# Kernel tuning notes

Hardware: AMD Instinct MI355X
Metric: run time of the kernel (lower is better)

The kernel has to match this reference:

```python
import jax, jax.numpy as jnp
import numpy as np

B, S, D = 2, 1024, 1024
E = 8          # routed experts
I = 1024       # per-expert intermediate
IS = 1024      # shared expert intermediate
TOP_K = 2
NUM_SHARED = 1


def setup_inputs() -> dict:
    key = jax.random.key(0)
    ks = jax.random.split(key, 8)
    scale = 0.02
    return {
        "x": jax.random.normal(ks[0], (B, S, D), dtype=jnp.float32),
        "w_gate": jax.random.normal(ks[1], (D, E), dtype=jnp.float32) * scale,
        "wg": jax.random.normal(ks[2], (E, D, I), dtype=jnp.float32) * scale,  # expert gate_proj
        "wu": jax.random.normal(ks[3], (E, D, I), dtype=jnp.float32) * scale,  # expert up_proj
        "wd": jax.random.normal(ks[4], (E, I, D), dtype=jnp.float32) * scale,  # expert down_proj
        "ws_g": jax.random.normal(ks[5], (NUM_SHARED, D, IS), dtype=jnp.float32) * scale,
        "ws_u": jax.random.normal(ks[6], (NUM_SHARED, D, IS), dtype=jnp.float32) * scale,
        "ws_d": jax.random.normal(ks[7], (NUM_SHARED, IS, D), dtype=jnp.float32) * scale,
    }


def _swiglu(t, w_gate_proj, w_up, w_down):
    # t: [N, D]
    g = t @ w_gate_proj            # [N, I]
    u = t @ w_up                   # [N, I]
    return (jax.nn.silu(g) * u) @ w_down  # [N, D]


def reference(x, w_gate, wg, wu, wd, ws_g, ws_u, ws_d):
    Bb, Ss, Dd = x.shape
    x_flat = x.reshape(Bb * Ss, Dd)                  # [N, D]
    N = x_flat.shape[0]

    # --- router ---
    logits = x_flat @ w_gate                          # [N, E]
    topk_logits, topk_idx = jax.lax.top_k(logits, TOP_K)
    topk_w = jax.nn.softmax(topk_logits, axis=-1)     # [N, K]

    # --- aux load-balancing loss ---
    one_hot = jax.nn.one_hot(topk_idx, E, dtype=jnp.float32)  # [N, K, E]
    f = one_hot.sum(axis=1).mean(axis=0)                       # [E]
    P = jax.nn.softmax(logits, axis=-1).mean(axis=0)           # [E]
    aux_loss = E * jnp.sum(f * P)

    # --- combine weights: cw[n, e] = sum_k topk_w[n,k] * 1[topk_idx[n,k]==e] ---
    cw = jnp.einsum("nk,nke->ne", topk_w, one_hot)             # [N, E]

    # --- routed experts: dense compute over all experts, weighted combine ---
    g = jnp.einsum("nd,edi->eni", x_flat, wg)                  # [E, N, I]
    u = jnp.einsum("nd,edi->eni", x_flat, wu)                  # [E, N, I]
    a = jax.nn.silu(g) * u                                     # [E, N, I]
    y = jnp.einsum("eni,eid->end", a, wd)                      # [E, N, D]
    routed = jnp.einsum("ne,end->nd", cw, y)                   # [N, D]

    # --- shared experts ---
    shared = jnp.zeros_like(x_flat)
    for s in range(NUM_SHARED):
        shared = shared + _swiglu(x_flat, ws_g[s], ws_u[s], ws_d[s])

    out = (routed + shared).reshape(Bb, Ss, Dd)
    return out, aux_loss
```

## Files before the change

kernel.cpp:

```cpp
#include <hip/hip_runtime.h>
#include <math.h>

typedef unsigned short u16;
typedef __attribute__((ext_vector_type(8))) short short8;
typedef __attribute__((ext_vector_type(4))) float f32x4;
typedef __attribute__((ext_vector_type(4))) unsigned short u16x4;
typedef __attribute__((ext_vector_type(8))) unsigned short u16x8;

#define N_TOK 2048
#define DIM 1024
#define OUT_ELEMS 2097152

#define GLDS16(gp, lp) __builtin_amdgcn_global_load_lds( \
    (const __attribute__((address_space(1))) unsigned int*)(gp), \
    (__attribute__((address_space(3))) unsigned int*)(lp), 16, 0, 0)

__device__ __forceinline__ u16 f2bf(float f) {
    union { float f; unsigned u; } v; v.f = f;
    unsigned r = (v.u + 0x7FFFu + ((v.u >> 16) & 1u)) >> 16;
    return (u16)r;
}
__device__ __forceinline__ float bf2f(u16 h) {
    union { unsigned u; float f; } v; v.u = ((unsigned)h) << 16;
    return v.f;
}

__device__ __forceinline__ void cvt_chunk(const float* __restrict__ src,
                                          u16* __restrict__ dst, int chunk,
                                          char* smem, int t) {
    float* tile = (float*)smem;
    const char* gsrc = (const char*)(src + (size_t)chunk * 8192);
    u16* dchunk = dst + (size_t)chunk * 8192;
    int w = t >> 6, l = t & 63;
#pragma unroll
    for (int j = 0; j < 8; j++) {
        int idx = w * 8 + j;
        GLDS16(gsrc + idx * 1024 + l * 16, smem + idx * 1024);
    }
    __syncthreads();
    int n0 = (t & 63) * 4 + (t >> 6) * 256;
    f32x4 v[8];
#pragma unroll
    for (int k = 0; k < 8; k++)
        v[k] = *(const f32x4*)(tile + k * 1024 + n0);
#pragma unroll
    for (int i = 0; i < 4; i++) {
        u16x8 o;
#pragma unroll
        for (int k = 0; k < 8; k++) o[k] = f2bf(v[k][i]);
        *(u16x8*)(dchunk + (size_t)(n0 + i) * 8) = o;
    }
}

__global__ __launch_bounds__(256)
void k_front(const float* __restrict__ wg, const float* __restrict__ wu,
             const float* __restrict__ wsg, const float* __restrict__ wsu,
             u16* __restrict__ wgt, u16* __restrict__ wut,
             u16* __restrict__ wsgt, u16* __restrict__ wsut,
             const float* __restrict__ x, const float* __restrict__ wgate,
             u16* __restrict__ xb, int* __restrict__ tidx, float* __restrict__ tw,
             float* __restrict__ Pp, int* __restrict__ Cp,
             int* __restrict__ tlist, int* __restrict__ curs) {
    __shared__ __attribute__((aligned(128))) char smem[32768];
    int bx = blockIdx.x;
    int t = threadIdx.x;
    if (bx < 2304) {
        int mat = bx >> 7, chunk = bx & 127;
        const float* src; u16* dst;
        if      (mat <  8) { src = wg + (size_t)mat * 1048576;       dst = wgt + (size_t)mat * 1048576; }
        else if (mat < 16) { src = wu + (size_t)(mat - 8) * 1048576; dst = wut + (size_t)(mat - 8) * 1048576; }
        else if (mat == 16){ src = wsg; dst = wsgt; }
        else               { src = wsu; dst = wsut; }
        cvt_chunk(src, dst, chunk, smem, t);
        return;
    }
    int b = bx - 2304;
    float* sP = (float*)smem;
    int*   sC = (int*)(smem + 64);
    if (t < 8) { sP[t] = 0.f; sC[t] = 0; }
    if (b == 0 && t < 16) curs[t] = 0;
    __syncthreads();
    int wave = t >> 6;
    int lane = t & 63;
    int n = b * 4 + wave;
    const float* xr = x + (size_t)n * DIM;
    u16* xbr = xb + (size_t)n * DIM;
    float acc[8] = {0.f,0.f,0.f,0.f,0.f,0.f,0.f,0.f};
#pragma unroll
    for (int i = 0; i < 16; i++) {
        int d = lane + i * 64;
        float xv = xr[d];
        xbr[d] = f2bf(xv);
        const float* wr = wgate + d * 8;
#pragma unroll
        for (int e = 0; e < 8; e++) acc[e] += xv * wr[e];
    }
#pragma unroll
    for (int off = 32; off; off >>= 1) {
#pragma unroll
        for (int e = 0; e < 8; e++) acc[e] += __shfl_xor(acc[e], off);
    }
    if (lane == 0) {
        tlist[4096 + n] = n;
        float mx = acc[0];
#pragma unroll
        for (int e = 1; e < 8; e++) mx = fmaxf(mx, acc[e]);
        float p[8], s = 0.f;
#pragma unroll
        for (int e = 0; e < 8; e++) { p[e] = expf(acc[e] - mx); s += p[e]; }
        float inv = 1.f / s;
#pragma unroll
        for (int e = 0; e < 8; e++) atomicAdd(&sP[e], p[e] * inv);
        int i0 = 0; float b0 = acc[0];
#pragma unroll
        for (int e = 1; e < 8; e++) if (acc[e] > b0) { b0 = acc[e]; i0 = e; }
        int i1 = -1; float b1 = -3.4e38f;
#pragma unroll
        for (int e = 0; e < 8; e++) if (e != i0 && acc[e] > b1) { b1 = acc[e]; i1 = e; }
        float w0 = 1.f / (1.f + expf(b1 - b0));
        tidx[n * 2] = i0; tidx[n * 2 + 1] = i1;
        tw[n * 2] = w0;   tw[n * 2 + 1] = 1.f - w0;
        atomicAdd(&sC[i0], 1);
        atomicAdd(&sC[i1], 1);
    }
    __syncthreads();
    if (t < 8) { Pp[b * 8 + t] = sP[t]; Cp[b * 8 + t] = sC[t]; }
}

__global__ void k_scatter(const int* __restrict__ tidx, const float* __restrict__ Pp,
                          const int* __restrict__ Cp, int* __restrict__ curs,
                          int* __restrict__ tlist, int* __restrict__ slots,
                          float* __restrict__ out, int* __restrict__ counts,
                          int* __restrict__ offs) {
    __shared__ int   s_off[8];
    __shared__ int   sCnt[8];
    __shared__ float sPs[8];
    __shared__ int   redC[256];
    __shared__ float redP[256];
    int t = threadIdx.x;
    int e = t & 7, g = t >> 3;
    int cs = 0; float ps = 0.f;
#pragma unroll
    for (int j = 0; j < 16; j++) {
        int b = g + j * 32;
        cs += Cp[b * 8 + e];
        ps += Pp[b * 8 + e];
    }
    redC[t] = cs; redP[t] = ps;
    __syncthreads();
    if (t < 8) {
        int c = 0; float p = 0.f;
        for (int g2 = 0; g2 < 32; g2++) { c += redC[g2 * 8 + t]; p += redP[g2 * 8 + t]; }
        sCnt[t] = c; sPs[t] = p;
    }
    __syncthreads();
    if (t == 0) {
        int o = 0;
        for (int e2 = 0; e2 < 8; e2++) { s_off[e2] = o; o += sCnt[e2]; }
    }
    __syncthreads();
    if (blockIdx.x == 0 && t == 0) {
        float aux = 0.f;
        for (int e2 = 0; e2 < 8; e2++) {
            aux += (float)sCnt[e2] * sPs[e2];
            offs[e2] = s_off[e2]; counts[e2] = sCnt[e2];
        }
        out[OUT_ELEMS] = 8.f * aux / ((float)N_TOK * (float)N_TOK);
        offs[8] = 4096; counts[8] = 2048;
    }
    int n = blockIdx.x * 256 + t;
    if (n < N_TOK) {
#pragma unroll
        for (int k = 0; k < 2; k++) {
            int ee = tidx[n * 2 + k];
            int p = atomicAdd(&curs[ee], 1);
            int sl = s_off[ee] + p;
            tlist[sl] = n;
            slots[n * 2 + k] = sl;
        }
    }
}

__global__ __launch_bounds__(256, 2)
void k_gemm1(const u16* __restrict__ xb, const u16* __restrict__ wgt,
             const u16* __restrict__ wut, const u16* __restrict__ wsgt,
             const u16* __restrict__ wsut, const int* __restrict__ tlist,
             const int* __restrict__ counts, const int* __restrict__ offs,
             u16* __restrict__ H,
             const float* __restrict__ wd, const float* __restrict__ wsd,
             u16* __restrict__ wdt, u16* __restrict__ wsdt) {
    __shared__ __attribute__((aligned(128))) char smem[49152];
    int bx = blockIdx.x;
    int t = threadIdx.x;
    if (bx < 1152) {
        int mat = bx >> 7, chunk = bx & 127;
        const float* src = (mat < 8) ? (wd + (size_t)mat * 1048576) : wsd;
        u16* dst = (mat < 8) ? (wdt + (size_t)mat * 1048576) : wsdt;
        cvt_chunk(src, dst, chunk, smem, t);
        return;
    }
    int bg = bx - 1152;
    int job = bg >> 7;
    int mt = (bg >> 3) & 15;
    int nt = bg & 7;
    int jcnt = counts[job];
    int m0 = mt << 7;
    if (m0 >= jcnt) return;
    int joff = offs[job];
    int n0 = nt << 7;
    const u16* Bg = (job < 8) ? (wgt + (size_t)job * 1048576) : wsgt;
    const u16* Bu = (job < 8) ? (wut + (size_t)job * 1048576) : wsut;

    int wave = t >> 6, lane = t & 63;
    int ch = (lane & 3) * 8;
    int r0 = (wave * 2 + 0) * 16 + (lane >> 2);
    int r1 = (wave * 2 + 1) * 16 + (lane >> 2);
    int tok0 = tlist[joff + m0 + r0];
    int tok1 = tlist[joff + m0 + r1];
    const u16* a0 = xb + (size_t)tok0 * 1024 + ch;
    const u16* a1 = xb + (size_t)tok1 * 1024 + ch;
    const u16* gB = Bg + (size_t)wave * 8192 + (size_t)(n0 + lane) * 8;
    const u16* uB = Bu + (size_t)wave * 8192 + (size_t)(n0 + lane) * 8;

    int wm = (wave >> 1) << 6, wn = (wave & 1) << 6;
    int quad = lane >> 4, lr = lane & 15;

    f32x4 accg[4][4], accu[4][4];
    f32x4 zz = {0.f, 0.f, 0.f, 0.f};
#pragma unroll
    for (int i = 0; i < 4; i++)
#pragma unroll
        for (int j = 0; j < 4; j++) { accg[i][j] = zz; accu[i][j] = zz; }

#define STAGE1(b_, s_) do { \
        char* bb = smem + (b_) * 24576; \
        u16* As_  = (u16*)bb; \
        u16* Bgs_ = (u16*)(bb + 8192); \
        u16* Bus_ = (u16*)(bb + 16384); \
        int k0_ = (s_) * 32; \
        size_t koff_ = (size_t)k0_ * 1024; \
        GLDS16(a0 + k0_, As_ + (wave * 2 + 0) * 512); \
        GLDS16(a1 + k0_, As_ + (wave * 2 + 1) * 512); \
        GLDS16(gB + koff_,       Bgs_ + wave * 1024); \
        GLDS16(gB + koff_ + 512, Bgs_ + wave * 1024 + 512); \
        GLDS16(uB + koff_,       Bus_ + wave * 1024); \
        GLDS16(uB + koff_ + 512, Bus_ + wave * 1024 + 512); \
    } while (0)

    STAGE1(0, 0);
    __syncthreads();
    for (int s = 0; s < 32; s++) {
        int cur = s & 1;
        if (s < 31) STAGE1(cur ^ 1, s + 1);
        const char* cb = smem + cur * 24576;
        const u16* Asr = (const u16*)cb;
        const u16* Bgr = (const u16*)(cb + 8192);
        const u16* Bur = (const u16*)(cb + 16384);
        short8 af[4], bgf[4], buf[4];
#pragma unroll
        for (int i = 0; i < 4; i++) {
            int nrow = wn + i * 16 + lr;
            af[i]  = *(const short8*)(Asr + (wm + i * 16 + lr) * 32 + quad * 8);
            bgf[i] = *(const short8*)(Bgr + quad * 1024 + nrow * 8);
            buf[i] = *(const short8*)(Bur + quad * 1024 + nrow * 8);
        }
#pragma unroll
        for (int mi = 0; mi < 4; mi++)
#pragma unroll
            for (int ni = 0; ni < 4; ni++) {
                accg[mi][ni] = __builtin_amdgcn_mfma_f32_16x16x32_bf16(af[mi], bgf[ni], accg[mi][ni], 0, 0, 0);
                accu[mi][ni] = __builtin_amdgcn_mfma_f32_16x16x32_bf16(af[mi], buf[ni], accu[mi][ni], 0, 0, 0);
            }
        __syncthreads();
    }
#undef STAGE1
#pragma unroll
    for (int mi = 0; mi < 4; mi++) {
        int rowb = m0 + wm + mi * 16 + quad * 4;
#pragma unroll
        for (int rr = 0; rr < 4; rr++) {
            int row = rowb + rr;
            if (row < jcnt) {
                size_t base = (size_t)(joff + row) * 1024 + n0 + wn;
#pragma unroll
                for (int ni = 0; ni < 4; ni++) {
                    float g = accg[mi][ni][rr];
                    float u = accu[mi][ni][rr];
                    float h = (g / (1.f + expf(-g))) * u;
                    H[base + ni * 16 + lr] = f2bf(h);
                }
            }
        }
    }
}

__global__ __launch_bounds__(256, 2)
void k_gemm2(const u16* __restrict__ H, const u16* __restrict__ wdt,
             const u16* __restrict__ wsdt, const int* __restrict__ counts,
             const int* __restrict__ offs, u16* __restrict__ Y) {
    __shared__ __attribute__((aligned(128))) char smem[32768];
    int bx = blockIdx.x;
    int job = bx >> 7;
    int mt = (bx >> 3) & 15;
    int nt = bx & 7;
    int jcnt = counts[job];
    int m0 = mt << 7;
    if (m0 >= jcnt) return;
    int joff = offs[job];
    int n0 = nt << 7;
    const u16* Bt = (job < 8) ? (wdt + (size_t)job * 1048576) : wsdt;

    int t = threadIdx.x;
    int wave = t >> 6, lane = t & 63;
    int ch = (lane & 3) * 8;
    int r0 = (wave * 2 + 0) * 16 + (lane >> 2);
    int r1 = (wave * 2 + 1) * 16 + (lane >> 2);
    const u16* a0 = H + (size_t)(joff + m0 + r0) * 1024 + ch;
    const u16* a1 = H + (size_t)(joff + m0 + r1) * 1024 + ch;
    const u16* bB = Bt + (size_t)wave * 8192 + (size_t)(n0 + lane) * 8;

    int wm = (wave >> 1) << 6, wn = (wave & 1) << 6;
    int quad = lane >> 4, lr = lane & 15;

    f32x4 acc[4][4];
    f32x4 zz = {0.f, 0.f, 0.f, 0.f};
#pragma unroll
    for (int i = 0; i < 4; i++)
#pragma unroll
        for (int j = 0; j < 4; j++) acc[i][j] = zz;

#define STAGE2(b_, s_) do { \
        char* bb = smem + (b_) * 16384; \
        u16* As_ = (u16*)bb; \
        u16* Bs_ = (u16*)(bb + 8192); \
        int k0_ = (s_) * 32; \
        size_t koff_ = (size_t)k0_ * 1024; \
        GLDS16(a0 + k0_, As_ + (wave * 2 + 0) * 512); \
        GLDS16(a1 + k0_, As_ + (wave * 2 + 1) * 512); \
        GLDS16(bB + koff_,       Bs_ + wave * 1024); \
        GLDS16(bB + koff_ + 512, Bs_ + wave * 1024 + 512); \
    } while (0)

    STAGE2(0, 0);
    __syncthreads();
    for (int s = 0; s < 32; s++) {
        int cur = s & 1;
        if (s < 31) STAGE2(cur ^ 1, s + 1);
        const char* cb = smem + cur * 16384;
        const u16* Asr = (const u16*)cb;
        const u16* Bsr = (const u16*)(cb + 8192);
        short8 af[4], bf[4];
#pragma unroll
        for (int i = 0; i < 4; i++) {
            af[i] = *(const short8*)(Asr + (wm + i * 16 + lr) * 32 + quad * 8);
            bf[i] = *(const short8*)(Bsr + quad * 1024 + (wn + i * 16 + lr) * 8);
        }
#pragma unroll
        for (int mi = 0; mi < 4; mi++)
#pragma unroll
            for (int ni = 0; ni < 4; ni++)
                acc[mi][ni] = __builtin_amdgcn_mfma_f32_16x16x32_bf16(af[mi], bf[ni], acc[mi][ni], 0, 0, 0);
        __syncthreads();
    }
#undef STAGE2
#pragma unroll
    for (int mi = 0; mi < 4; mi++) {
        int rowb = m0 + wm + mi * 16 + quad * 4;
#pragma unroll
        for (int rr = 0; rr < 4; rr++) {
            int row = rowb + rr;
            if (row < jcnt) {
                u16* yrow = Y + (size_t)(joff + row) * 1024 + n0 + wn;
#pragma unroll
                for (int ni = 0; ni < 4; ni++)
                    yrow[ni * 16 + lr] = f2bf(acc[mi][ni][rr]);
            }
        }
    }
}

__global__ void k_combine(const u16* __restrict__ Y, const int* __restrict__ slots,
                          const float* __restrict__ tw, float* __restrict__ out) {
    int n = blockIdx.x;
    int d = threadIdx.x;
    int s0 = slots[n * 2], s1 = slots[n * 2 + 1];
    float w0 = tw[n * 2], w1 = tw[n * 2 + 1];
    u16x4 y0 = ((const u16x4*)(Y + (size_t)s0 * 1024))[d];
    u16x4 y1 = ((const u16x4*)(Y + (size_t)s1 * 1024))[d];
    u16x4 ys = ((const u16x4*)(Y + (size_t)(4096 + n) * 1024))[d];
    f32x4 r;
    r.x = w0 * bf2f(y0.x) + w1 * bf2f(y1.x) + bf2f(ys.x);
    r.y = w0 * bf2f(y0.y) + w1 * bf2f(y1.y) + bf2f(ys.y);
    r.z = w0 * bf2f(y0.z) + w1 * bf2f(y1.z) + bf2f(ys.z);
    r.w = w0 * bf2f(y0.w) + w1 * bf2f(y1.w) + bf2f(ys.w);
    ((f32x4*)(out + (size_t)n * 1024))[d] = r;
}

extern "C" void kernel_launch(void* const* d_in, const int* in_sizes, int n_in,
                              void* d_out, int out_size, void* d_ws, size_t ws_size,
                              hipStream_t stream) {
    const float* x     = (const float*)d_in[0];
    const float* wgate = (const float*)d_in[1];
    const float* wg    = (const float*)d_in[2];
    const float* wu    = (const float*)d_in[3];
    const float* wd    = (const float*)d_in[4];
    const float* wsg   = (const float*)d_in[5];
    const float* wsu   = (const float*)d_in[6];
    const float* wsd   = (const float*)d_in[7];
    float* out = (float*)d_out;

    char* ws = (char*)d_ws;
    u16*   xb    = (u16*)(ws + 0);
    u16*   wgt   = (u16*)(ws + 4194304);
    u16*   wut   = (u16*)(ws + 20971520);
    u16*   wdt   = (u16*)(ws + 37748736);
    u16*   wsgt  = (u16*)(ws + 54525952);
    u16*   wsut  = (u16*)(ws + 56623104);
    u16*   wsdt  = (u16*)(ws + 58720256);
    u16*   H     = (u16*)(ws + 60817408);
    u16*   Y     = (u16*)(ws + 4194304);
    int*   tidx  = (int*)(ws + 73400320);
    float* tw    = (float*)(ws + 73416704);
    int*   tlist = (int*)(ws + 73433088);
    int*   slots = (int*)(ws + 73457664);
    int*   counts= (int*)(ws + 73474048);
    int*   offs  = (int*)(ws + 73474112);
    int*   curs  = (int*)(ws + 73474176);
    float* Pp    = (float*)(ws + 73474304);
    int*   Cp    = (int*)(ws + 73490688);

    k_front<<<2816, 256, 0, stream>>>(wg, wu, wsg, wsu, wgt, wut, wsgt, wsut,
                                      x, wgate, xb, tidx, tw, Pp, Cp, tlist, curs);
    k_scatter<<<8, 256, 0, stream>>>(tidx, Pp, Cp, curs, tlist, slots,
                                     out, counts, offs);
    k_gemm1<<<2304, 256, 0, stream>>>(xb, wgt, wut, wsgt, wsut, tlist, counts, offs,
                                      H, wd, wsd, wdt, wsdt);
    k_gemm2<<<1152, 256, 0, stream>>>(H, wdt, wsdt, counts, offs, Y);
    k_combine<<<2048, 256, 0, stream>>>(Y, slots, tw, out);
}
```

Before: 260.9 us.

## Fuse all stages into one cooperative persistent kernel with grid syncs

Replaces the five separate launches (router/convert, scatter, gemm1+convert, gemm2, combine) with a single cooperative kernel of 768 persistent blocks that loops over the same job lists and separates stages with grid.sync. It also reorders gemm tile mapping so shared-expert tiles come first and routed tiles are interleaved by M-tile across experts. The aim is to remove launch gaps and tail effects between kernels. The cost is grid-wide barriers, 48KB LDS at 3 blocks per CU, and a fallback to the old launches if the cooperative launch fails.

```diff
diff --git a/kernel.cpp b/kernel.cpp
--- a/kernel.cpp
+++ b/kernel.cpp
@@ -1,5 +1,8 @@
 #include <hip/hip_runtime.h>
+#include <hip/hip_cooperative_groups.h>
 #include <math.h>
+
+namespace cg = cooperative_groups;
 
 typedef unsigned short u16;
 typedef __attribute__((ext_vector_type(8))) short short8;
@@ -52,29 +55,31 @@
     }
 }
 
-__global__ __launch_bounds__(256)
-void k_front(const float* __restrict__ wg, const float* __restrict__ wu,
-             const float* __restrict__ wsg, const float* __restrict__ wsu,
-             u16* __restrict__ wgt, u16* __restrict__ wut,
-             u16* __restrict__ wsgt, u16* __restrict__ wsut,
-             const float* __restrict__ x, const float* __restrict__ wgate,
-             u16* __restrict__ xb, int* __restrict__ tidx, float* __restrict__ tw,
-             float* __restrict__ Pp, int* __restrict__ Cp,
-             int* __restrict__ tlist, int* __restrict__ curs) {
-    __shared__ __attribute__((aligned(128))) char smem[32768];
-    int bx = blockIdx.x;
-    int t = threadIdx.x;
-    if (bx < 2304) {
-        int mat = bx >> 7, chunk = bx & 127;
-        const float* src; u16* dst;
-        if      (mat <  8) { src = wg + (size_t)mat * 1048576;       dst = wgt + (size_t)mat * 1048576; }
-        else if (mat < 16) { src = wu + (size_t)(mat - 8) * 1048576; dst = wut + (size_t)(mat - 8) * 1048576; }
-        else if (mat == 16){ src = wsg; dst = wsgt; }
-        else               { src = wsu; dst = wsut; }
-        cvt_chunk(src, dst, chunk, smem, t);
-        return;
-    }
-    int b = bx - 2304;
+__device__ __forceinline__ void cvt_gu_job(int j, const float* wg, const float* wu,
+                                           const float* wsg, const float* wsu,
+                                           u16* wgt, u16* wut, u16* wsgt, u16* wsut,
+                                           char* smem, int t) {
+    int mat = j >> 7, chunk = j & 127;
+    const float* src; u16* dst;
+    if      (mat <  8) { src = wg + (size_t)mat * 1048576;       dst = wgt + (size_t)mat * 1048576; }
+    else if (mat < 16) { src = wu + (size_t)(mat - 8) * 1048576; dst = wut + (size_t)(mat - 8) * 1048576; }
+    else if (mat == 16){ src = wsg; dst = wsgt; }
+    else               { src = wsu; dst = wsut; }
+    cvt_chunk(src, dst, chunk, smem, t);
+}
+
+__device__ __forceinline__ void cvt_d_job(int j, const float* wd, const float* wsd,
+                                          u16* wdt, u16* wsdt, char* smem, int t) {
+    int mat = j >> 7, chunk = j & 127;
+    const float* src = (mat < 8) ? (wd + (size_t)mat * 1048576) : wsd;
+    u16* dst = (mat < 8) ? (wdt + (size_t)mat * 1048576) : wsdt;
+    cvt_chunk(src, dst, chunk, smem, t);
+}
+
+__device__ __forceinline__ void router_job(int b, const float* x, const float* wgate,
+                                           u16* xb, int* tidx, float* tw,
+                                           float* Pp, int* Cp, int* tlist,
+                                           int* curs, char* smem, int t) {
     float* sP = (float*)smem;
     int*   sC = (int*)(smem + 64);
     if (t < 8) { sP[t] = 0.f; sC[t] = 0; }
@@ -127,17 +132,15 @@
     if (t < 8) { Pp[b * 8 + t] = sP[t]; Cp[b * 8 + t] = sC[t]; }
 }
 
-__global__ void k_scatter(const int* __restrict__ tidx, const float* __restrict__ Pp,
-                          const int* __restrict__ Cp, int* __restrict__ curs,
-                          int* __restrict__ tlist, int* __restrict__ slots,
-                          float* __restrict__ out, int* __restrict__ counts,
-                          int* __restrict__ offs) {
-    __shared__ int   s_off[8];
-    __shared__ int   sCnt[8];
-    __shared__ float sPs[8];
-    __shared__ int   redC[256];
-    __shared__ float redP[256];
-    int t = threadIdx.x;
+__device__ __forceinline__ void scatter_job(int bid, const int* tidx, const float* Pp,
+                                            const int* Cp, int* curs, int* tlist,
+                                            int* slots, float* out, int* counts,
+                                            int* offs, char* smem, int t) {
+    int*   s_off = (int*)smem;
+    int*   sCnt  = (int*)(smem + 32);
+    float* sPs   = (float*)(smem + 64);
+    int*   redC  = (int*)(smem + 128);
+    float* redP  = (float*)(smem + 1152);
     int e = t & 7, g = t >> 3;
     int cs = 0; float ps = 0.f;
 #pragma unroll
@@ -159,7 +162,7 @@
         for (int e2 = 0; e2 < 8; e2++) { s_off[e2] = o; o += sCnt[e2]; }
     }
     __syncthreads();
-    if (blockIdx.x == 0 && t == 0) {
+    if (bid == 0 && t == 0) {
         float aux = 0.f;
         for (int e2 = 0; e2 < 8; e2++) {
             aux += (float)sCnt[e2] * sPs[e2];
@@ -168,7 +171,7 @@
         out[OUT_ELEMS] = 8.f * aux / ((float)N_TOK * (float)N_TOK);
         offs[8] = 4096; counts[8] = 2048;
     }
-    int n = blockIdx.x * 256 + t;
+    int n = bid * 256 + t;
     if (n < N_TOK) {
 #pragma unroll
         for (int k = 0; k < 2; k++) {
@@ -181,28 +184,24 @@
     }
 }
 
-__global__ __launch_bounds__(256, 2)
-void k_gemm1(const u16* __restrict__ xb, const u16* __restrict__ wgt,
-             const u16* __restrict__ wut, const u16* __restrict__ wsgt,
-             const u16* __restrict__ wsut, const int* __restrict__ tlist,
-             const int* __restrict__ counts, const int* __restrict__ offs,
-             u16* __restrict__ H,
-             const float* __restrict__ wd, const float* __restrict__ wsd,
-             u16* __restrict__ wdt, u16* __restrict__ wsdt) {
-    __shared__ __attribute__((aligned(128))) char smem[49152];
-    int bx = blockIdx.x;
-    int t = threadIdx.x;
-    if (bx < 1152) {
-        int mat = bx >> 7, chunk = bx & 127;
-        const float* src = (mat < 8) ? (wd + (size_t)mat * 1048576) : wsd;
-        u16* dst = (mat < 8) ? (wdt + (size_t)mat * 1048576) : wsdt;
-        cvt_chunk(src, dst, chunk, smem, t);
-        return;
-    }
-    int bg = bx - 1152;
-    int job = bg >> 7;
-    int mt = (bg >> 3) & 15;
-    int nt = bg & 7;
+__device__ __forceinline__ void gemm_map(int jj, int& job, int& mt, int& nt) {
+    if (jj < 128) { job = 8; mt = jj >> 3; nt = jj & 7; }
+    else {
+        int r = jj - 128;
+        mt = r >> 6;
+        int rem = r & 63;
+        job = rem >> 3;
+        nt = rem & 7;
+    }
+}
+
+__device__ __forceinline__ void gemm1_job(
+    int jj, const u16* __restrict__ xb, const u16* __restrict__ wgt,
+    const u16* __restrict__ wut, const u16* __restrict__ wsgt,
+    const u16* __restrict__ wsut, const int* __restrict__ tlist,
+    const int* __restrict__ counts, const int* __restrict__ offs,
+    u16* __restrict__ H, char* smem, int t) {
+    int job, mt, nt; gemm_map(jj, job, mt, nt);
     int jcnt = counts[job];
     int m0 = mt << 7;
     if (m0 >= jcnt) return;
@@ -294,15 +293,11 @@
     }
 }
 
-__global__ __launch_bounds__(256, 2)
-void k_gemm2(const u16* __restrict__ H, const u16* __restrict__ wdt,
-             const u16* __restrict__ wsdt, const int* __restrict__ counts,
-             const int* __restrict__ offs, u16* __restrict__ Y) {
-    __shared__ __attribute__((aligned(128))) char smem[32768];
-    int bx = blockIdx.x;
-    int job = bx >> 7;
-    int mt = (bx >> 3) & 15;
-    int nt = bx & 7;
+__device__ __forceinline__ void gemm2_job(
+    int jj, const u16* __restrict__ H, const u16* __restrict__ wdt,
+    const u16* __restrict__ wsdt, const int* __restrict__ counts,
+    const int* __restrict__ offs, u16* __restrict__ Y, char* smem, int t) {
+    int job, mt, nt; gemm_map(jj, job, mt, nt);
     int jcnt = counts[job];
     int m0 = mt << 7;
     if (m0 >= jcnt) return;
@@ -310,7 +305,6 @@
     int n0 = nt << 7;
     const u16* Bt = (job < 8) ? (wdt + (size_t)job * 1048576) : wsdt;
 
-    int t = threadIdx.x;
     int wave = t >> 6, lane = t & 63;
     int ch = (lane & 3) * 8;
     int r0 = (wave * 2 + 0) * 16 + (lane >> 2);
@@ -379,21 +373,110 @@
     }
 }
 
-__global__ void k_combine(const u16* __restrict__ Y, const int* __restrict__ slots,
-                          const float* __restrict__ tw, float* __restrict__ out) {
-    int n = blockIdx.x;
-    int d = threadIdx.x;
+__device__ __forceinline__ void combine_job(int n, const u16* __restrict__ Y,
+                                            const int* __restrict__ slots,
+                                            const float* __restrict__ tw,
+                                            float* __restrict__ out, int t) {
     int s0 = slots[n * 2], s1 = slots[n * 2 + 1];
     float w0 = tw[n * 2], w1 = tw[n * 2 + 1];
-    u16x4 y0 = ((const u16x4*)(Y + (size_t)s0 * 1024))[d];
-    u16x4 y1 = ((const u16x4*)(Y + (size_t)s1 * 1024))[d];
-    u16x4 ys = ((const u16x4*)(Y + (size_t)(4096 + n) * 1024))[d];
+    u16x4 y0 = ((const u16x4*)(Y + (size_t)s0 * 1024))[t];
+    u16x4 y1 = ((const u16x4*)(Y + (size_t)s1 * 1024))[t];
+    u16x4 ys = ((const u16x4*)(Y + (size_t)(4096 + n) * 1024))[t];
     f32x4 r;
     r.x = w0 * bf2f(y0.x) + w1 * bf2f(y1.x) + bf2f(ys.x);
     r.y = w0 * bf2f(y0.y) + w1 * bf2f(y1.y) + bf2f(ys.y);
     r.z = w0 * bf2f(y0.z) + w1 * bf2f(y1.z) + bf2f(ys.z);
     r.w = w0 * bf2f(y0.w) + w1 * bf2f(y1.w) + bf2f(ys.w);
-    ((f32x4*)(out + (size_t)n * 1024))[d] = r;
+    ((f32x4*)(out + (size_t)n * 1024))[t] = r;
+}
+
+__global__ __launch_bounds__(256, 3)
+void k_mega(const float* x, const float* wgate, const float* wg, const float* wu,
+            const float* wd, const float* wsg, const float* wsu, const float* wsd,
+            float* out, u16* xb, u16* wgt, u16* wut, u16* wdt, u16* wsgt,
+            u16* wsut, u16* wsdt, u16* H, u16* Y, int* tidx, float* tw,
+            int* tlist, int* slots, int* counts, int* offs, int* curs,
+            float* Pp, int* Cp) {
+    cg::grid_group grid = cg::this_grid();
+    __shared__ __attribute__((aligned(128))) char smem[49152];
+    int bid = blockIdx.x;
+    int t = threadIdx.x;
+    const int NB = (int)gridDim.x;
+
+    for (int j = bid; j < 2816; j += NB) {
+        __syncthreads();
+        if (j < 512) router_job(j, x, wgate, xb, tidx, tw, Pp, Cp, tlist, curs, smem, t);
+        else         cvt_gu_job(j - 512, wg, wu, wsg, wsu, wgt, wut, wsgt, wsut, smem, t);
+    }
+    grid.sync();
+    if (bid < 8)
+        scatter_job(bid, tidx, Pp, Cp, curs, tlist, slots, out, counts, offs, smem, t);
+    grid.sync();
+    for (int j = bid; j < 2304; j += NB) {
+        __syncthreads();
+        if (j < 1152) gemm1_job(j, xb, wgt, wut, wsgt, wsut, tlist, counts, offs, H, smem, t);
+        else          cvt_d_job(j - 1152, wd, wsd, wdt, wsdt, smem, t);
+    }
+    grid.sync();
+    for (int j = bid; j < 1152; j += NB) {
+        __syncthreads();
+        gemm2_job(j, H, wdt, wsdt, counts, offs, Y, smem, t);
+    }
+    grid.sync();
+    for (int n = bid; n < 2048; n += NB)
+        combine_job(n, Y, slots, tw, out, t);
+}
+
+__global__ __launch_bounds__(256)
+void k_front(const float* __restrict__ wg, const float* __restrict__ wu,
+             const float* __restrict__ wsg, const float* __restrict__ wsu,
+             u16* __restrict__ wgt, u16* __restrict__ wut,
+             u16* __restrict__ wsgt, u16* __restrict__ wsut,
+             const float* __restrict__ x, const float* __restrict__ wgate,
+             u16* __restrict__ xb, int* __restrict__ tidx, float* __restrict__ tw,
+             float* __restrict__ Pp, int* __restrict__ Cp,
+             int* __restrict__ tlist, int* __restrict__ curs) {
+    __shared__ __attribute__((aligned(128))) char smem[32768];
+    int bx = blockIdx.x, t = threadIdx.x;
+    if (bx < 512) router_job(bx, x, wgate, xb, tidx, tw, Pp, Cp, tlist, curs, smem, t);
+    else          cvt_gu_job(bx - 512, wg, wu, wsg, wsu, wgt, wut, wsgt, wsut, smem, t);
+}
+
+__global__ void k_scatter(const int* __restrict__ tidx, const float* __restrict__ Pp,
+                          const int* __restrict__ Cp, int* __restrict__ curs,
+                          int* __restrict__ tlist, int* __restrict__ slots,
+                          float* __restrict__ out, int* __restrict__ counts,
+                          int* __restrict__ offs) {
+    __shared__ __attribute__((aligned(128))) char smem[4096];
+    scatter_job(blockIdx.x, tidx, Pp, Cp, curs, tlist, slots, out, counts, offs,
+                smem, threadIdx.x);
+}
+
+__global__ __launch_bounds__(256, 2)
+void k_gemm1(const u16* __restrict__ xb, const u16* __restrict__ wgt,
+             const u16* __restrict__ wut, const u16* __restrict__ wsgt,
+             const u16* __restrict__ wsut, const int* __restrict__ tlist,
+             const int* __restrict__ counts, const int* __restrict__ offs,
+             u16* __restrict__ H,
+             const float* __restrict__ wd, const float* __restrict__ wsd,
+             u16* __restrict__ wdt, u16* __restrict__ wsdt) {
+    __shared__ __attribute__((aligned(128))) char smem[49152];
+    int bx = blockIdx.x, t = threadIdx.x;
+    if (bx < 1152) gemm1_job(bx, xb, wgt, wut, wsgt, wsut, tlist, counts, offs, H, smem, t);
+    else           cvt_d_job(bx - 1152, wd, wsd, wdt, wsdt, smem, t);
+}
+
+__global__ __launch_bounds__(256, 2)
+void k_gemm2(const u16* __restrict__ H, const u16* __restrict__ wdt,
+             const u16* __restrict__ wsdt, const int* __restrict__ counts,
+             const int* __restrict__ offs, u16* __restrict__ Y) {
+    __shared__ __attribute__((aligned(128))) char smem[32768];
+    gemm2_job(blockIdx.x, H, wdt, wsdt, counts, offs, Y, smem, threadIdx.x);
+}
+
+__global__ void k_combine(const u16* __restrict__ Y, const int* __restrict__ slots,
+                          const float* __restrict__ tw, float* __restrict__ out) {
+    combine_job(blockIdx.x, Y, slots, tw, out, threadIdx.x);
 }
 
 extern "C" void kernel_launch(void* const* d_in, const int* in_sizes, int n_in,
@@ -429,6 +512,15 @@
     float* Pp    = (float*)(ws + 73474304);
     int*   Cp    = (int*)(ws + 73490688);
 
+    void* args[] = { &x, &wgate, &wg, &wu, &wd, &wsg, &wsu, &wsd, &out,
+                     &xb, &wgt, &wut, &wdt, &wsgt, &wsut, &wsdt, &H, &Y,
+                     &tidx, &tw, &tlist, &slots, &counts, &offs, &curs,
+                     &Pp, &Cp };
+    hipError_t err = hipLaunchCooperativeKernel((const void*)k_mega, dim3(768),
+                                                dim3(256), args, 0, stream);
+    if (err == hipSuccess) return;
+    (void)hipGetLastError();
+
     k_front<<<2816, 256, 0, stream>>>(wg, wu, wsg, wsu, wgt, wut, wsgt, wsut,
                                       x, wgate, xb, tidx, tw, Pp, Cp, tlist, curs);
     k_scatter<<<8, 256, 0, stream>>>(tidx, Pp, Cp, curs, tlist, slots,
```

Result: slower. 698.1 us (+167.6%).
